# Optimization experiments

Measured on AMD Instinct MI355X. Metric: run time of the kernel, lower is better.

## Reference

```python
import jax, jax.numpy as jnp
from jax import lax
import numpy as np

# NOTE: the original module calls an opaque CUDA 'approximate dot-product' conv kernel.
# Its backward uses EXACT conv2d gradients for input/weight, so the reference forward
# math is the exact conv2d the kernel approximates. `approximate` is a learned scalar
# controlling the hardware approximation level; it does not change the exact-math output.

STRIDE = 1
PAD = (1, 1)  # (padH, padW)


def setup_inputs() -> dict:
    key = jax.random.key(0)
    k1, k2, k3 = jax.random.split(key, 3)
    B, Cin, H, W = 32, 128, 56, 56
    Cout, K = 256, 3
    x = jax.random.normal(k1, (B, Cin, H, W), dtype=jnp.float32)
    # weight init: uniform(-1, 1) per reset_parameters
    weight = jax.random.uniform(k2, (Cout, Cin, K, K), dtype=jnp.float32, minval=-1.0, maxval=1.0)
    fan_in = Cin * K * K
    bound = 1.0 / np.sqrt(fan_in)
    bias = jax.random.uniform(k3, (Cout,), dtype=jnp.float32, minval=-bound, maxval=bound)
    approximate = jnp.ones((1,), dtype=jnp.float32)
    return {"x": x, "weight": weight, "bias": bias, "approximate": approximate}


def reference(x, weight, bias, approximate):
    # Exact conv2d, NCHW input, OIHW kernel. `approximate` controls only the
    # hardware approximation level in the original CUDA kernel.
    out = lax.conv_general_dilated(
        x, weight,
        window_strides=(STRIDE, STRIDE),
        padding=((PAD[0], PAD[0]), (PAD[1], PAD[1])),
        dimension_numbers=("NCHW", "OIHW", "NCHW"),
    )
    return out + bias.reshape(1, -1, 1, 1)
```

## Files before the change

### kernel.cpp

```cpp
#include <hip/hip_runtime.h>


typedef __attribute__((ext_vector_type(8))) short short8;
typedef __attribute__((ext_vector_type(4))) float floatx4;

typedef __attribute__((address_space(1))) const void* gas_ptr;
typedef __attribute__((address_space(3))) void* las_ptr;

__device__ static inline void gl2lds16(const void* g, void* l) {
    __builtin_amdgcn_global_load_lds((gas_ptr)g, (las_ptr)l, 16, 0, 0);
}

__device__ static inline float bf2f(unsigned short u) {
    union { unsigned int i; float f; } x; x.i = ((unsigned int)u) << 16; return x.f;
}
__device__ static inline unsigned short f2bf(float f) {
    union { float f; unsigned int i; } x; x.f = f;
    unsigned int r = (x.i + 0x7FFFu + ((x.i >> 16) & 1u)) >> 16;
    return (unsigned short)r;
}

__global__ void detect_dtype(const unsigned int* __restrict__ x,
                             unsigned int* __restrict__ flag) {
    int cnt = 0;
    for (int r = 0; r < 4; ++r) {
        unsigned int w = x[r * 64 + threadIdx.x];
        unsigned short lo = (unsigned short)(w & 0xFFFFu);
        int e = (lo >> 7) & 0xFF;
        bool plaus = (lo == 0) || (e >= 96 && e <= 144);
        unsigned long long b = __ballot(plaus);
        if (threadIdx.x == 0) cnt += (int)__popcll(b);
    }
    if (threadIdx.x == 0) *flag = (cnt >= 205) ? 1u : 0u;
}

__global__ void wt_repack(const void* __restrict__ wsrc,
                          unsigned short* __restrict__ wt,
                          const unsigned int* __restrict__ flag) {
    const bool isbf = (*flag != 0);
    int idx = blockIdx.x * 256 + threadIdx.x;
    int ci  = idx & 127;
    int co  = (idx >> 7) & 255;
    int off = idx >> 15;
    size_t s = (size_t)(co * 128 + ci) * 9 + off;
    float v = isbf ? bf2f(((const unsigned short*)wsrc)[s])
                   : ((const float*)wsrc)[s];
    wt[idx] = f2bf(v);
}

__global__ __launch_bounds__(256) void x_repack(
    const void* __restrict__ xsrc, unsigned short* __restrict__ xp,
    const unsigned int* __restrict__ flag) {
    __shared__ unsigned short tile[56 * 130];
    const bool isbf = (*flag != 0);
    const int bh  = blockIdx.x;
    const int b   = bh / 58, hp = bh - b * 58;
    const int tid = threadIdx.x;
    unsigned short* row = xp + (size_t)(b * 58 + hp) * 58 * 128;
    if (hp == 0 || hp == 57) {
        uint4 z; z.x = z.y = z.z = z.w = 0u;
        uint4* r = (uint4*)row;
        for (int t = tid; t < 928; t += 256) r[t] = z;
        return;
    }
    const int h = hp - 1;
    if (isbf) {
        const unsigned short* xs =
            (const unsigned short*)xsrc + (size_t)b * 128 * 3136 + h * 56;
#pragma unroll
        for (int it = 0; it < 7; ++it) {
            int idx = it * 256 + tid;
            int ci = idx / 14, w4 = idx - ci * 14;
            ushort4 v = *(const ushort4*)(xs + (size_t)ci * 3136 + w4 * 4);
            tile[(w4 * 4 + 0) * 130 + ci] = v.x;
            tile[(w4 * 4 + 1) * 130 + ci] = v.y;
            tile[(w4 * 4 + 2) * 130 + ci] = v.z;
            tile[(w4 * 4 + 3) * 130 + ci] = v.w;
        }
    } else {
        const float* xs = (const float*)xsrc + (size_t)b * 128 * 3136 + h * 56;
#pragma unroll
        for (int it = 0; it < 7; ++it) {
            int idx = it * 256 + tid;
            int ci = idx / 14, w4 = idx - ci * 14;
            float4 v = *(const float4*)(xs + (size_t)ci * 3136 + w4 * 4);
            tile[(w4 * 4 + 0) * 130 + ci] = f2bf(v.x);
            tile[(w4 * 4 + 1) * 130 + ci] = f2bf(v.y);
            tile[(w4 * 4 + 2) * 130 + ci] = f2bf(v.z);
            tile[(w4 * 4 + 3) * 130 + ci] = f2bf(v.w);
        }
    }
    __syncthreads();
#pragma unroll
    for (int it = 0; it < 4; ++it) {
        int k = it * 256 + tid;
        if (k >= 928) break;
        int wq = k >> 4, cc = k & 15;
        uint4 v;
        if (wq == 0 || wq == 57) { v.x = v.y = v.z = v.w = 0u; }
        else {
            const unsigned short* p = &tile[(wq - 1) * 130 + cc * 8];
            union { unsigned short s[8]; uint4 u; } pk;
#pragma unroll
            for (int j = 0; j < 8; ++j) pk.s[j] = p[j];
            v = pk.u;
        }
        *(uint4*)(row + wq * 128 + cc * 8) = v;
    }
}

__global__ __launch_bounds__(384) void conv_mfma(
    const unsigned short* __restrict__ xp,
    const unsigned short* __restrict__ wt,
    const void* __restrict__ bias,
    void* __restrict__ out,
    const unsigned int* __restrict__ flag)
{
    __shared__ __align__(16) char lds[65536];
    __shared__ unsigned ready[4];
    __shared__ unsigned freed[4];
    const bool isbf = (*flag != 0);
    const int tid   = threadIdx.x;
    const int lane  = tid & 63;
    const int wv    = tid >> 6;
    const int ntile = blockIdx.x;
    const int mtile = blockIdx.y;

    if (tid < 4) { ready[tid] = 0u; freed[tid] = 0u; }
    __syncthreads();

    if (wv >= 4) {
        const int pid = wv - 4;
        const int srp = lane >> 2;
        const int clg = (lane & 3) ^ ((lane >> 3) & 3);
        const unsigned short* aB = wt + (mtile * 128 + srp) * 128 + clg * 8;
        size_t bRow[8];
#pragma unroll
        for (int i = 0; i < 8; ++i) {
            const int n = ntile * 128 + i * 16 + srp;
            const int b = n / 3136, s2 = n - b * 3136;
            const int h = s2 / 56,  w = s2 - h * 56;
            bRow[i] = ((size_t)(b * 58 + h) * 58 + w) * 128 + clg * 8;
        }
        for (int s = pid; s < 36; s += 2) {
            const int bf_ = s & 3, cyc = s >> 2;
            if (cyc > 0) {
                const unsigned gate = 4u * (unsigned)cyc;
                while (__hip_atomic_load(&freed[bf_], __ATOMIC_ACQUIRE,
                                         __HIP_MEMORY_SCOPE_WORKGROUP) < gate)
                    __builtin_amdgcn_s_sleep(1);
            }
            char* buf = lds + bf_ * 16384;
            const int off = s >> 2, kb = (s & 3) << 5;
            const int dh = off / 3, dw = off - dh * 3;
            const int aoff = off * 32768 + kb;
            const int boff = (dh * 58 + dw) * 128 + kb;
#pragma unroll
            for (int i = 0; i < 8; ++i)
                gl2lds16(aB + i * 2048 + aoff, buf + i * 1024);
#pragma unroll
            for (int i = 0; i < 8; ++i)
                gl2lds16(xp + bRow[i] + boff, buf + 8192 + i * 1024);
            __builtin_amdgcn_s_waitcnt(0x3F70);
            if (lane == 0)
                __hip_atomic_store(&ready[bf_], (unsigned)(s + 1),
                                   __ATOMIC_RELEASE, __HIP_MEMORY_SCOPE_WORKGROUP);
        }
        return;
    }

    const int mbase = (wv >> 1) * 64 + (lane & 15);
    const int nbase = (wv & 1) * 64 + (lane & 15);
    const int ph    = (lane >> 4) ^ (((lane & 15) >> 1) & 3);
    floatx4 acc[4][4] = {};

#pragma unroll 4
    for (int s = 0; s < 36; ++s) {
        const int bf_ = s & 3;
        while (__hip_atomic_load(&ready[bf_], __ATOMIC_ACQUIRE,
                                 __HIP_MEMORY_SCOPE_WORKGROUP) < (unsigned)(s + 1))
            ;
        const char* la = lds + bf_ * 16384;
        const char* lb = la + 8192;
        short8 af[4], bfr[4];
#pragma unroll
        for (int t = 0; t < 4; ++t) {
            af[t]  = *(const short8*)(la + (mbase + t * 16) * 64 + ph * 16);
            bfr[t] = *(const short8*)(lb + (nbase + t * 16) * 64 + ph * 16);
        }
#pragma unroll
        for (int i = 0; i < 4; ++i)
#pragma unroll
            for (int j = 0; j < 4; ++j)
                acc[i][j] = __builtin_amdgcn_mfma_f32_16x16x32_bf16(
                    af[i], bfr[j], acc[i][j], 0, 0, 0);
        if (lane == 0)
            __hip_atomic_fetch_add(&freed[bf_], 1u, __ATOMIC_RELEASE,
                                   __HIP_MEMORY_SCOPE_WORKGROUP);
    }

    const int q = lane >> 4;
#pragma unroll
    for (int j = 0; j < 4; ++j) {
        const int n = ntile * 128 + (wv & 1) * 64 + j * 16 + (lane & 15);
        const int b = n / 3136;
        const int s = n - b * 3136;
#pragma unroll
        for (int i = 0; i < 4; ++i) {
            const int co = mtile * 128 + (wv >> 1) * 64 + i * 16 + q * 4;
            float bv[4];
            if (isbf) {
                const ushort4 bb = *(const ushort4*)((const unsigned short*)bias + co);
                bv[0] = bf2f(bb.x); bv[1] = bf2f(bb.y);
                bv[2] = bf2f(bb.z); bv[3] = bf2f(bb.w);
            } else {
                const float4 bb = *(const float4*)((const float*)bias + co);
                bv[0] = bb.x; bv[1] = bb.y; bv[2] = bb.z; bv[3] = bb.w;
            }
#pragma unroll
            for (int r = 0; r < 4; ++r) {
                const float v = acc[i][j][r] + bv[r];
                const size_t o = (size_t)b * 802816 + (size_t)(co + r) * 3136 + s;
                if (isbf) ((unsigned short*)out)[o] = f2bf(v);
                else      ((float*)out)[o] = v;
            }
        }
    }
}

__global__ void conv_naive(const float* __restrict__ x,
                           const float* __restrict__ w,
                           const float* __restrict__ bias,
                           float* __restrict__ out) {
    long long i = (long long)blockIdx.x * 256 + threadIdx.x;
    if (i >= 25690112LL) return;
    int wo = (int)(i % 56); long long t = i / 56;
    int ho = (int)(t % 56); t /= 56;
    int co = (int)(t % 256); int b = (int)(t / 256);
    float acc = bias[co];
    for (int ci = 0; ci < 128; ++ci)
        for (int dh = 0; dh < 3; ++dh) {
            int hi = ho + dh - 1; if ((unsigned)hi >= 56u) continue;
            for (int dw = 0; dw < 3; ++dw) {
                int wi = wo + dw - 1; if ((unsigned)wi >= 56u) continue;
                acc += x[((size_t)(b * 128 + ci) * 56 + hi) * 56 + wi] *
                       w[((co * 128 + ci) * 3 + dh) * 3 + dw];
            }
        }
    out[i] = acc;
}

extern "C" void kernel_launch(void* const* d_in, const int* in_sizes, int n_in,
                              void* d_out, int out_size, void* d_ws, size_t ws_size,
                              hipStream_t stream) {
    const void* x    = d_in[0];
    const void* w    = d_in[1];
    const void* bias = d_in[2];

    const size_t xp_bytes = (size_t)32 * 58 * 58 * 128 * 2;
    const size_t wt_off   = xp_bytes;
    const size_t wt_bytes = (size_t)9 * 256 * 128 * 2;
    const size_t fl_off   = wt_off + wt_bytes;
    const size_t need     = fl_off + 64;

    if (ws_size >= need) {
        unsigned short* xp = (unsigned short*)d_ws;
        unsigned short* wt = (unsigned short*)((char*)d_ws + wt_off);
        unsigned int* flag = (unsigned int*)((char*)d_ws + fl_off);
        detect_dtype<<<1, 64, 0, stream>>>((const unsigned int*)x, flag);
        x_repack<<<32 * 58, 256, 0, stream>>>(x, xp, flag);
        wt_repack<<<1152, 256, 0, stream>>>(w, wt, flag);
        dim3 grid(784, 2, 1);
        conv_mfma<<<grid, 384, 0, stream>>>(xp, wt, bias, d_out, flag);
    } else {
        conv_naive<<<(25690112 + 255) / 256, 256, 0, stream>>>(
            (const float*)x, (const float*)w, (const float*)bias, (float*)d_out);
    }
}
```

Before: 244.3 us.

## Inline dtype detection per wave and shrink LDS ring to three buffers

Removes the separate detect_dtype launch and its flag buffer by having each wave run the bf16-plausibility ballot on the input pointer itself. The conv kernel's LDS ring goes from four 16KB stages to three (48KB), with producer and consumer indexing changed to mod-3 rotation. The smaller LDS footprint is meant to let more workgroups share a CU, and dropping a kernel launch cuts fixed overhead. The cost is shallower prefetch depth, plus redundant detection loads in every block and wave.

After: 224.7 us. 1.09x faster.

```diff
diff --git a/kernel.cpp b/kernel.cpp
--- a/kernel.cpp
+++ b/kernel.cpp
@@ -20,24 +20,23 @@
     return (unsigned short)r;
 }
 
-__global__ void detect_dtype(const unsigned int* __restrict__ x,
-                             unsigned int* __restrict__ flag) {
+__device__ static inline bool wave_detect_bf16(const unsigned int* __restrict__ p) {
+    const int lane = threadIdx.x & 63;
     int cnt = 0;
+#pragma unroll
     for (int r = 0; r < 4; ++r) {
-        unsigned int w = x[r * 64 + threadIdx.x];
+        unsigned int w = p[r * 64 + lane];
         unsigned short lo = (unsigned short)(w & 0xFFFFu);
         int e = (lo >> 7) & 0xFF;
         bool plaus = (lo == 0) || (e >= 96 && e <= 144);
-        unsigned long long b = __ballot(plaus);
-        if (threadIdx.x == 0) cnt += (int)__popcll(b);
-    }
-    if (threadIdx.x == 0) *flag = (cnt >= 205) ? 1u : 0u;
+        cnt += (int)__popcll(__ballot(plaus));
+    }
+    return cnt >= 205;
 }
 
 __global__ void wt_repack(const void* __restrict__ wsrc,
-                          unsigned short* __restrict__ wt,
-                          const unsigned int* __restrict__ flag) {
-    const bool isbf = (*flag != 0);
+                          unsigned short* __restrict__ wt) {
+    const bool isbf = wave_detect_bf16((const unsigned int*)wsrc);
     int idx = blockIdx.x * 256 + threadIdx.x;
     int ci  = idx & 127;
     int co  = (idx >> 7) & 255;
@@ -49,10 +48,8 @@
 }
 
 __global__ __launch_bounds__(256) void x_repack(
-    const void* __restrict__ xsrc, unsigned short* __restrict__ xp,
-    const unsigned int* __restrict__ flag) {
+    const void* __restrict__ xsrc, unsigned short* __restrict__ xp) {
     __shared__ unsigned short tile[56 * 130];
-    const bool isbf = (*flag != 0);
     const int bh  = blockIdx.x;
     const int b   = bh / 58, hp = bh - b * 58;
     const int tid = threadIdx.x;
@@ -63,6 +60,7 @@
         for (int t = tid; t < 928; t += 256) r[t] = z;
         return;
     }
+    const bool isbf = wave_detect_bf16((const unsigned int*)xsrc);
     const int h = hp - 1;
     if (isbf) {
         const unsigned short* xs =
@@ -114,19 +112,18 @@
     const unsigned short* __restrict__ wt,
     const void* __restrict__ bias,
     void* __restrict__ out,
-    const unsigned int* __restrict__ flag)
+    const void* __restrict__ xorig)
 {
-    __shared__ __align__(16) char lds[65536];
-    __shared__ unsigned ready[4];
-    __shared__ unsigned freed[4];
-    const bool isbf = (*flag != 0);
+    __shared__ __align__(16) char lds[49152];
+    __shared__ unsigned ready[3];
+    __shared__ unsigned freed[3];
     const int tid   = threadIdx.x;
     const int lane  = tid & 63;
     const int wv    = tid >> 6;
     const int ntile = blockIdx.x;
     const int mtile = blockIdx.y;
 
-    if (tid < 4) { ready[tid] = 0u; freed[tid] = 0u; }
+    if (tid < 3) { ready[tid] = 0u; freed[tid] = 0u; }
     __syncthreads();
 
     if (wv >= 4) {
@@ -142,10 +139,10 @@
             const int h = s2 / 56,  w = s2 - h * 56;
             bRow[i] = ((size_t)(b * 58 + h) * 58 + w) * 128 + clg * 8;
         }
+        int bf_ = pid;
         for (int s = pid; s < 36; s += 2) {
-            const int bf_ = s & 3, cyc = s >> 2;
-            if (cyc > 0) {
-                const unsigned gate = 4u * (unsigned)cyc;
+            if (s >= 3) {
+                const unsigned gate = 4u * (unsigned)(s / 3);
                 while (__hip_atomic_load(&freed[bf_], __ATOMIC_ACQUIRE,
                                          __HIP_MEMORY_SCOPE_WORKGROUP) < gate)
                     __builtin_amdgcn_s_sleep(1);
@@ -165,18 +162,20 @@
             if (lane == 0)
                 __hip_atomic_store(&ready[bf_], (unsigned)(s + 1),
                                    __ATOMIC_RELEASE, __HIP_MEMORY_SCOPE_WORKGROUP);
+            bf_ += 2; if (bf_ >= 3) bf_ -= 3;
         }
         return;
     }
 
+    const bool isbf = wave_detect_bf16((const unsigned int*)xorig);
     const int mbase = (wv >> 1) * 64 + (lane & 15);
     const int nbase = (wv & 1) * 64 + (lane & 15);
     const int ph    = (lane >> 4) ^ (((lane & 15) >> 1) & 3);
     floatx4 acc[4][4] = {};
 
-#pragma unroll 4
+#pragma unroll 3
     for (int s = 0; s < 36; ++s) {
-        const int bf_ = s & 3;
+        const int bf_ = s % 3;
         while (__hip_atomic_load(&ready[bf_], __ATOMIC_ACQUIRE,
                                  __HIP_MEMORY_SCOPE_WORKGROUP) < (unsigned)(s + 1))
             ;
@@ -260,18 +259,15 @@
     const size_t xp_bytes = (size_t)32 * 58 * 58 * 128 * 2;
     const size_t wt_off   = xp_bytes;
     const size_t wt_bytes = (size_t)9 * 256 * 128 * 2;
-    const size_t fl_off   = wt_off + wt_bytes;
-    const size_t need     = fl_off + 64;
+    const size_t need     = wt_off + wt_bytes;
 
     if (ws_size >= need) {
         unsigned short* xp = (unsigned short*)d_ws;
         unsigned short* wt = (unsigned short*)((char*)d_ws + wt_off);
-        unsigned int* flag = (unsigned int*)((char*)d_ws + fl_off);
-        detect_dtype<<<1, 64, 0, stream>>>((const unsigned int*)x, flag);
-        x_repack<<<32 * 58, 256, 0, stream>>>(x, xp, flag);
-        wt_repack<<<1152, 256, 0, stream>>>(w, wt, flag);
+        x_repack<<<32 * 58, 256, 0, stream>>>(x, xp);
+        wt_repack<<<1152, 256, 0, stream>>>(w, wt);
         dim3 grid(784, 2, 1);
-        conv_mfma<<<grid, 384, 0, stream>>>(xp, wt, bias, d_out, flag);
+        conv_mfma<<<grid, 384, 0, stream>>>(xp, wt, bias, d_out, x);
     } else {
         conv_naive<<<(25690112 + 255) / 256, 256, 0, stream>>>(
             (const float*)x, (const float*)w, (const float*)bias, (float*)d_out);
```
